# Kernel optimization log

Measured on AMD Instinct MI355X. Metric: run time of the kernel, lower is better.

The kernel has to match this reference:

```python
import jax, jax.numpy as jnp
import numpy as np

M, K, N = 8192, 4096, 12288


def setup_inputs() -> dict:
    key = jax.random.key(0)
    k1, k2, k3, k4 = jax.random.split(key, 4)
    input_tensor = jax.random.normal(k1, (1, M, K), dtype=jnp.float32)
    # int8 quantized weight [N, K] and per-output-channel scale [N, 1]
    weight = jax.random.randint(k2, (N, K), -127, 128, dtype=jnp.int32).astype(jnp.int8)
    weight_scale = (jax.random.uniform(k3, (N, 1), dtype=jnp.float32) * 0.01 + 1e-4)
    bias = jax.random.normal(k4, (N,), dtype=jnp.float32) * 0.1
    return {"input_tensor": input_tensor, "weight": weight,
            "weight_scale": weight_scale, "bias": bias}


def reference(input_tensor, weight, weight_scale, bias):
    x = input_tensor[0]  # squeeze(0) -> [M, K]
    # dynamic per-token symmetric int8 quantization: scale = absmax/127
    a_scale = jnp.max(jnp.abs(x), axis=-1, keepdims=True) / 127.0  # [M, 1]
    q = jnp.clip(jnp.round(x / a_scale), -128.0, 127.0)  # int8 values held in f32
    # int8 GEMM accumulated (emulated in f32), then dequant with per-token x per-channel scales
    acc = jnp.einsum('mk,nk->mn', q, weight.astype(jnp.float32))  # [M, N]
    out = acc * a_scale * weight_scale[:, 0][None, :] + bias[None, :]
    return out[None].astype(input_tensor.dtype)  # unsqueeze(0) -> [1, M, N]
```

## Files before the change

### kernel.cpp

```cpp
#include <hip/hip_runtime.h>
#include <cstdint>

#define M_DIM 8192
#define K_DIM 4096
#define N_DIM 12288
#define KT 64

using i32x4 = __attribute__((ext_vector_type(4))) int;

__device__ inline void gload_lds16(const void* g, void* l) {
    __builtin_amdgcn_global_load_lds(
        (const __attribute__((address_space(1))) void*)g,
        (__attribute__((address_space(3))) void*)l,
        16, 0, 0);
}

__global__ __launch_bounds__(256) void quant_pack(const float* __restrict__ x,
                                                  const int* __restrict__ w32,
                                                  int8_t* __restrict__ qa,
                                                  float* __restrict__ ascale,
                                                  int8_t* __restrict__ wq) {
    const int t = threadIdx.x;
    if (blockIdx.x < M_DIM) {
        const int row = blockIdx.x;
        const float4* xr = (const float4*)(x + (size_t)row * K_DIM);
        float4 v[4];
        float amax = 0.0f;
#pragma unroll
        for (int c = 0; c < 4; ++c) {
            v[c] = xr[t + 256 * c];
            amax = fmaxf(amax, fmaxf(fmaxf(fabsf(v[c].x), fabsf(v[c].y)),
                                     fmaxf(fabsf(v[c].z), fabsf(v[c].w))));
        }
#pragma unroll
        for (int off = 32; off > 0; off >>= 1)
            amax = fmaxf(amax, __shfl_xor(amax, off));
        __shared__ float smax[4];
        if ((t & 63) == 0) smax[t >> 6] = amax;
        __syncthreads();
        amax = fmaxf(fmaxf(smax[0], smax[1]), fmaxf(smax[2], smax[3]));
        const float sc = amax * (1.0f / 127.0f);
        const float inv = (amax > 0.0f) ? (127.0f / amax) : 0.0f;
        if (t == 0) ascale[row] = sc;

        int* q32 = (int*)(qa + (size_t)row * K_DIM);
#pragma unroll
        for (int c = 0; c < 4; ++c) {
            int q0 = (int)rintf(v[c].x * inv);
            int q1 = (int)rintf(v[c].y * inv);
            int q2 = (int)rintf(v[c].z * inv);
            int q3 = (int)rintf(v[c].w * inv);
            q0 = min(127, max(-128, q0));
            q1 = min(127, max(-128, q1));
            q2 = min(127, max(-128, q2));
            q3 = min(127, max(-128, q3));
            q32[t + 256 * c] = (q0 & 255) | ((q1 & 255) << 8) | ((q2 & 255) << 16) | (q3 << 24);
        }
    } else {
        const int pb = blockIdx.x - M_DIM;
        const size_t total4 = (size_t)N_DIM * K_DIM / 4;
        const size_t stride = (size_t)2048 * 256;
        int* out32 = (int*)wq;
        for (size_t i = (size_t)pb * 256 + t; i < total4; i += stride) {
            const int4 v = ((const int4*)w32)[i];
            out32[i] = (v.x & 255) | ((v.y & 255) << 8) | ((v.z & 255) << 16) | (v.w << 24);
        }
    }
}

__global__ __launch_bounds__(512, 2) void gemm_i8(const int8_t* __restrict__ qa,
                                                  const int8_t* __restrict__ wq,
                                                  const float* __restrict__ ascale,
                                                  const float* __restrict__ wscale,
                                                  const float* __restrict__ bias,
                                                  float* __restrict__ out) {
    __shared__ int8_t lds[4][2][16384];

    const int t = threadIdx.x;
    const int lane = t & 63;
    const int wave = t >> 6;
    const int wm = wave >> 2;
    const int wn = wave & 3;
    const int lrow = lane & 15;
    const int lk = lane >> 4;
    const int rslot = (lk ^ ((lrow >> 1) & 3)) << 4;

    const int flat = blockIdx.x;
    const int sw = (flat & 7) * 192 + (flat >> 3);
    const int bm = sw / 48;
    const int bn = sw % 48;

    const int g = (t & 3) ^ ((t >> 3) & 3);
    const size_t aoff0 = (size_t)(bm * 256 + (t >> 2)) * K_DIM + (size_t)g * 16;
    const size_t aoff1 = aoff0 + (size_t)128 * K_DIM;
    const size_t boff0 = (size_t)(bn * 256 + (t >> 2)) * K_DIM + (size_t)g * 16;
    const size_t boff1 = boff0 + (size_t)128 * K_DIM;

#define STAGE_A(sb, jt)                                                      \
    {                                                                        \
        gload_lds16(qa + aoff0 + (size_t)(jt) * 64, &lds[sb][0][t * 16]);    \
        gload_lds16(qa + aoff1 + (size_t)(jt) * 64,                          \
                    &lds[sb][0][t * 16 + 8192]);                             \
    }
#define STAGE_B(sb, jt)                                                      \
    {                                                                        \
        gload_lds16(wq + boff0 + (size_t)(jt) * 64, &lds[sb][1][t * 16]);    \
        gload_lds16(wq + boff1 + (size_t)(jt) * 64,                          \
                    &lds[sb][1][t * 16 + 8192]);                             \
    }

    i32x4 acc[8][4] = {};

#pragma unroll
    for (int p = 0; p < 3; ++p) {
        STAGE_A(p, p);
        STAGE_B(p, p);
    }

    for (int j = 0; j < KT; ++j) {
        const int cb = j & 3;
        const int pb = (j + 3) & 3;

        if (j + 3 < KT) {
            STAGE_A(pb, j + 3);
            asm volatile("s_waitcnt vmcnt(10)" ::: "memory");
        } else if (j + 2 < KT) {
            asm volatile("s_waitcnt vmcnt(8)" ::: "memory");
        } else if (j + 1 < KT) {
            asm volatile("s_waitcnt vmcnt(4)" ::: "memory");
        } else {
            asm volatile("s_waitcnt vmcnt(0)" ::: "memory");
        }
        __builtin_amdgcn_s_barrier();
        __builtin_amdgcn_sched_barrier(0);

        const int8_t* __restrict__ LA = lds[cb][0];
        const int8_t* __restrict__ LB = lds[cb][1];
        i32x4 af[4], bf[4], ah[4];
#pragma unroll
        for (int nf = 0; nf < 4; ++nf)
            bf[nf] = *(const i32x4*)&LB[(wn * 64 + nf * 16 + lrow) * 64 + rslot];
#pragma unroll
        for (int mf = 0; mf < 4; ++mf)
            af[mf] = *(const i32x4*)&LA[(wm * 128 + mf * 16 + lrow) * 64 + rslot];
        asm volatile("s_waitcnt lgkmcnt(0)" ::: "memory");
        __builtin_amdgcn_sched_barrier(0);
        __builtin_amdgcn_s_setprio(1);
#pragma unroll
        for (int mf = 0; mf < 4; ++mf)
#pragma unroll
            for (int nf = 0; nf < 4; ++nf)
                acc[mf][nf] = __builtin_amdgcn_mfma_i32_16x16x64_i8(
                    af[mf], bf[nf], acc[mf][nf], 0, 0, 0);
        __builtin_amdgcn_s_setprio(0);
        __builtin_amdgcn_s_barrier();

#pragma unroll
        for (int mf = 0; mf < 4; ++mf)
            ah[mf] = *(const i32x4*)&LA[(wm * 128 + (mf + 4) * 16 + lrow) * 64 + rslot];
        if (j + 3 < KT) STAGE_B(pb, j + 3);
        __builtin_amdgcn_s_barrier();
        asm volatile("s_waitcnt lgkmcnt(0)" ::: "memory");
        __builtin_amdgcn_sched_barrier(0);
        __builtin_amdgcn_s_setprio(1);
#pragma unroll
        for (int mf = 0; mf < 4; ++mf)
#pragma unroll
            for (int nf = 0; nf < 4; ++nf)
                acc[mf + 4][nf] = __builtin_amdgcn_mfma_i32_16x16x64_i8(
                    ah[mf], bf[nf], acc[mf + 4][nf], 0, 0, 0);
        __builtin_amdgcn_s_setprio(0);
        __builtin_amdgcn_s_barrier();
    }

    const int r0 = bm * 256 + wm * 128;
    const int c0 = bn * 256 + wn * 64;
    float asc[8][4];
#pragma unroll
    for (int m = 0; m < 8; ++m)
#pragma unroll
        for (int jj = 0; jj < 4; ++jj)
            asc[m][jj] = ascale[r0 + m * 16 + lk * 4 + jj];
#pragma unroll
    for (int n = 0; n < 4; ++n) {
        const int col = c0 + n * 16 + lrow;
        const float wsc = wscale[col];
        const float bb = bias[col];
#pragma unroll
        for (int m = 0; m < 8; ++m) {
#pragma unroll
            for (int jj = 0; jj < 4; ++jj) {
                const int row = r0 + m * 16 + lk * 4 + jj;
                out[(size_t)row * N_DIM + col] = (float)acc[m][n][jj] * asc[m][jj] * wsc + bb;
            }
        }
    }
}

extern "C" void kernel_launch(void* const* d_in, const int* in_sizes, int n_in,
                              void* d_out, int out_size, void* d_ws, size_t ws_size,
                              hipStream_t stream) {
    const float* x = (const float*)d_in[0];
    const int* w32 = (const int*)d_in[1];
    const float* wscale = (const float*)d_in[2];
    const float* bias = (const float*)d_in[3];
    float* out = (float*)d_out;

    int8_t* qa = (int8_t*)d_ws;
    float* ascale = (float*)((char*)d_ws + (size_t)M_DIM * K_DIM);
    int8_t* wq = (int8_t*)((char*)d_ws + (size_t)M_DIM * K_DIM +
                           (size_t)M_DIM * sizeof(float));

    quant_pack<<<M_DIM + 2048, 256, 0, stream>>>(x, w32, qa, ascale, wq);
    gemm_i8<<<1536, 512, 0, stream>>>(qa, wq, ascale, wscale, bias, out);
}
```

Baseline: 555.3 us.

## Double-buffer MFMA fragments in registers and prefetch next LDS tile during compute

Restructures the int8 GEMM main loop so the A and B fragments for the next K-tile are read from LDS into a second register set while the MFMAs run on the current set. All four global-to-LDS loads per tile are merged into one stage per iteration, and the loop is unrolled by two to alternate the register buffers. This cuts the barriers per K-step from four to one and hides LDS read latency behind MFMA work. The cost is more live VGPRs (two full 8x4 fragment sets alongside 128 accumulator registers), which under launch_bounds(512,2) risks spills or lower occupancy.

```diff
diff --git a/kernel.cpp b/kernel.cpp
--- a/kernel.cpp
+++ b/kernel.cpp
@@ -96,81 +96,71 @@
     const size_t boff0 = (size_t)(bn * 256 + (t >> 2)) * K_DIM + (size_t)g * 16;
     const size_t boff1 = boff0 + (size_t)128 * K_DIM;
 
-#define STAGE_A(sb, jt)                                                      \
-    {                                                                        \
-        gload_lds16(qa + aoff0 + (size_t)(jt) * 64, &lds[sb][0][t * 16]);    \
-        gload_lds16(qa + aoff1 + (size_t)(jt) * 64,                          \
-                    &lds[sb][0][t * 16 + 8192]);                             \
-    }
-#define STAGE_B(sb, jt)                                                      \
-    {                                                                        \
-        gload_lds16(wq + boff0 + (size_t)(jt) * 64, &lds[sb][1][t * 16]);    \
-        gload_lds16(wq + boff1 + (size_t)(jt) * 64,                          \
-                    &lds[sb][1][t * 16 + 8192]);                             \
+#define STAGE_ALL(sb, jt)                                                     \
+    {                                                                         \
+        gload_lds16(qa + aoff0 + (size_t)(jt) * 64, &lds[sb][0][t * 16]);     \
+        gload_lds16(qa + aoff1 + (size_t)(jt) * 64, &lds[sb][0][t * 16 + 8192]); \
+        gload_lds16(wq + boff0 + (size_t)(jt) * 64, &lds[sb][1][t * 16]);     \
+        gload_lds16(wq + boff1 + (size_t)(jt) * 64, &lds[sb][1][t * 16 + 8192]); \
     }
 
     i32x4 acc[8][4] = {};
-
-#pragma unroll
-    for (int p = 0; p < 3; ++p) {
-        STAGE_A(p, p);
-        STAGE_B(p, p);
-    }
-
-    for (int j = 0; j < KT; ++j) {
-        const int cb = j & 3;
-        const int pb = (j + 3) & 3;
-
-        if (j + 3 < KT) {
-            STAGE_A(pb, j + 3);
-            asm volatile("s_waitcnt vmcnt(10)" ::: "memory");
-        } else if (j + 2 < KT) {
-            asm volatile("s_waitcnt vmcnt(8)" ::: "memory");
-        } else if (j + 1 < KT) {
-            asm volatile("s_waitcnt vmcnt(4)" ::: "memory");
-        } else {
-            asm volatile("s_waitcnt vmcnt(0)" ::: "memory");
-        }
-        __builtin_amdgcn_s_barrier();
-        __builtin_amdgcn_sched_barrier(0);
-
-        const int8_t* __restrict__ LA = lds[cb][0];
-        const int8_t* __restrict__ LB = lds[cb][1];
-        i32x4 af[4], bf[4], ah[4];
+    i32x4 fa0[8], fb0[4], fa1[8], fb1[4];
+
+#pragma unroll
+    for (int p = 0; p < 3; ++p) STAGE_ALL(p, p);
+    asm volatile("s_waitcnt vmcnt(8)" ::: "memory");
+    __builtin_amdgcn_s_barrier();
+    __builtin_amdgcn_sched_barrier(0);
+    {
+        const int8_t* __restrict__ LA = lds[0][0];
+        const int8_t* __restrict__ LB = lds[0][1];
 #pragma unroll
         for (int nf = 0; nf < 4; ++nf)
-            bf[nf] = *(const i32x4*)&LB[(wn * 64 + nf * 16 + lrow) * 64 + rslot];
-#pragma unroll
-        for (int mf = 0; mf < 4; ++mf)
-            af[mf] = *(const i32x4*)&LA[(wm * 128 + mf * 16 + lrow) * 64 + rslot];
-        asm volatile("s_waitcnt lgkmcnt(0)" ::: "memory");
-        __builtin_amdgcn_sched_barrier(0);
-        __builtin_amdgcn_s_setprio(1);
-#pragma unroll
-        for (int mf = 0; mf < 4; ++mf)
-#pragma unroll
-            for (int nf = 0; nf < 4; ++nf)
-                acc[mf][nf] = __builtin_amdgcn_mfma_i32_16x16x64_i8(
-                    af[mf], bf[nf], acc[mf][nf], 0, 0, 0);
-        __builtin_amdgcn_s_setprio(0);
-        __builtin_amdgcn_s_barrier();
-
-#pragma unroll
-        for (int mf = 0; mf < 4; ++mf)
-            ah[mf] = *(const i32x4*)&LA[(wm * 128 + (mf + 4) * 16 + lrow) * 64 + rslot];
-        if (j + 3 < KT) STAGE_B(pb, j + 3);
-        __builtin_amdgcn_s_barrier();
-        asm volatile("s_waitcnt lgkmcnt(0)" ::: "memory");
-        __builtin_amdgcn_sched_barrier(0);
-        __builtin_amdgcn_s_setprio(1);
-#pragma unroll
-        for (int mf = 0; mf < 4; ++mf)
-#pragma unroll
-            for (int nf = 0; nf < 4; ++nf)
-                acc[mf + 4][nf] = __builtin_amdgcn_mfma_i32_16x16x64_i8(
-                    ah[mf], bf[nf], acc[mf + 4][nf], 0, 0, 0);
-        __builtin_amdgcn_s_setprio(0);
-        __builtin_amdgcn_s_barrier();
+            fb0[nf] = *(const i32x4*)&LB[(wn * 64 + nf * 16 + lrow) * 64 + rslot];
+#pragma unroll
+        for (int mf = 0; mf < 8; ++mf)
+            fa0[mf] = *(const i32x4*)&LA[(wm * 128 + mf * 16 + lrow) * 64 + rslot];
+    }
+
+#define ITER(J, CA, CB, NA, NB)                                               \
+    do {                                                                      \
+        if ((J) + 3 < KT) {                                                   \
+            STAGE_ALL(((J) + 3) & 3, (J) + 3);                                \
+            asm volatile("s_waitcnt vmcnt(8)" ::: "memory");                  \
+        } else if ((J) + 2 < KT) {                                            \
+            asm volatile("s_waitcnt vmcnt(4)" ::: "memory");                  \
+        } else if ((J) + 1 < KT) {                                            \
+            asm volatile("s_waitcnt vmcnt(0)" ::: "memory");                  \
+        }                                                                     \
+        __builtin_amdgcn_s_barrier();                                         \
+        __builtin_amdgcn_sched_barrier(0);                                    \
+        if ((J) + 1 < KT) {                                                   \
+            const int8_t* __restrict__ LA = lds[((J) + 1) & 3][0];            \
+            const int8_t* __restrict__ LB = lds[((J) + 1) & 3][1];            \
+            _Pragma("unroll")                                                 \
+            for (int nf = 0; nf < 4; ++nf)                                    \
+                NB[nf] = *(const i32x4*)&LB[(wn * 64 + nf * 16 + lrow) * 64 + rslot]; \
+            _Pragma("unroll")                                                 \
+            for (int mf = 0; mf < 8; ++mf)                                    \
+                NA[mf] = *(const i32x4*)&LA[(wm * 128 + mf * 16 + lrow) * 64 + rslot]; \
+        }                                                                     \
+        __builtin_amdgcn_sched_barrier(0);                                    \
+        __builtin_amdgcn_s_setprio(1);                                        \
+        _Pragma("unroll")                                                     \
+        for (int mf = 0; mf < 8; ++mf)                                        \
+            _Pragma("unroll")                                                 \
+            for (int nf = 0; nf < 4; ++nf)                                    \
+                acc[mf][nf] = __builtin_amdgcn_mfma_i32_16x16x64_i8(          \
+                    CA[mf], CB[nf], acc[mf][nf], 0, 0, 0);                    \
+        __builtin_amdgcn_s_setprio(0);                                        \
+        asm volatile("s_waitcnt lgkmcnt(0)" ::: "memory");                    \
+        __builtin_amdgcn_sched_barrier(0);                                    \
+    } while (0)
+
+    for (int j = 0; j < KT; j += 2) {
+        ITER(j, fa0, fb0, fa1, fb1);
+        ITER(j + 1, fa1, fb1, fa0, fb0);
     }
 
     const int r0 = bm * 256 + wm * 128;
```

Result: faster. 543.2 us (-2.2%).

## Switch int8 GEMM to K=128 tiles with double buffering and quadrant MFMA schedule

Applied to the files above, without the earlier changes.

Doubles the K-tile to 128 bytes and replaces the 4-stage, 64-wide LDS ring with a 2-stage double buffer of 128-wide tiles. It uses an 8-way XOR swizzle and splits each iteration into four quadrant MFMA phases that interleave LDS reads and global-to-LDS staging. The aim is fewer loop iterations and barriers per unit of K, and more MFMA work between synchronisations. In exchange, prefetch depth drops from three tiles to one, which may expose more global-memory latency.

```diff
diff --git a/kernel.cpp b/kernel.cpp
--- a/kernel.cpp
+++ b/kernel.cpp
@@ -4,7 +4,7 @@
 #define M_DIM 8192
 #define K_DIM 4096
 #define N_DIM 12288
-#define KT 64
+#define KT 32
 
 using i32x4 = __attribute__((ext_vector_type(4))) int;
 
@@ -74,7 +74,7 @@
                                                   const float* __restrict__ wscale,
                                                   const float* __restrict__ bias,
                                                   float* __restrict__ out) {
-    __shared__ int8_t lds[4][2][16384];
+    __shared__ int8_t lds[2][2][32768];
 
     const int t = threadIdx.x;
     const int lane = t & 63;
@@ -83,94 +83,95 @@
     const int wn = wave & 3;
     const int lrow = lane & 15;
     const int lk = lane >> 4;
-    const int rslot = (lk ^ ((lrow >> 1) & 3)) << 4;
+    const int sw7 = lrow & 7;
 
     const int flat = blockIdx.x;
     const int sw = (flat & 7) * 192 + (flat >> 3);
     const int bm = sw / 48;
     const int bn = sw % 48;
 
-    const int g = (t & 3) ^ ((t >> 3) & 3);
-    const size_t aoff0 = (size_t)(bm * 256 + (t >> 2)) * K_DIM + (size_t)g * 16;
-    const size_t aoff1 = aoff0 + (size_t)128 * K_DIM;
-    const size_t boff0 = (size_t)(bn * 256 + (t >> 2)) * K_DIM + (size_t)g * 16;
-    const size_t boff1 = boff0 + (size_t)128 * K_DIM;
-
-#define STAGE_A(sb, jt)                                                      \
-    {                                                                        \
-        gload_lds16(qa + aoff0 + (size_t)(jt) * 64, &lds[sb][0][t * 16]);    \
-        gload_lds16(qa + aoff1 + (size_t)(jt) * 64,                          \
-                    &lds[sb][0][t * 16 + 8192]);                             \
-    }
-#define STAGE_B(sb, jt)                                                      \
-    {                                                                        \
-        gload_lds16(wq + boff0 + (size_t)(jt) * 64, &lds[sb][1][t * 16]);    \
-        gload_lds16(wq + boff1 + (size_t)(jt) * 64,                          \
-                    &lds[sb][1][t * 16 + 8192]);                             \
-    }
+    const int srow = t >> 3;
+    const int g = (t & 7) ^ (srow & 7);
+
+#define STAGE_OP(ptr, sb, op, rowbase, jt)                                     \
+    {                                                                          \
+        _Pragma("unroll") for (int c = 0; c < 4; ++c)                          \
+            gload_lds16(ptr + (size_t)((rowbase) + srow + 64 * c) * K_DIM +    \
+                            (size_t)g * 16 + (size_t)(jt) * 128,               \
+                        &lds[sb][op][c * 8192 + t * 16]);                      \
+    }
+
+#define READ_A(dst, LA, mh)                                                    \
+    {                                                                          \
+        _Pragma("unroll") for (int mf = 0; mf < 4; ++mf)                       \
+            _Pragma("unroll") for (int ks = 0; ks < 2; ++ks)                   \
+                dst[mf][ks] = *(const i32x4*)&LA[(wm * 128 + (mh)*64 +         \
+                                                 mf * 16 + lrow) * 128 +       \
+                                                ((((ks << 2) | lk) ^ sw7) << 4)]; \
+    }
+#define READ_B(dst, LB, nh)                                                    \
+    {                                                                          \
+        _Pragma("unroll") for (int nf = 0; nf < 2; ++nf)                       \
+            _Pragma("unroll") for (int ks = 0; ks < 2; ++ks)                   \
+                dst[nf][ks] = *(const i32x4*)&LB[(wn * 64 + (nh)*32 +          \
+                                                 nf * 16 + lrow) * 128 +       \
+                                                ((((ks << 2) | lk) ^ sw7) << 4)]; \
+    }
+#define MM(AH, BH, mh, nh)                                                     \
+    {                                                                          \
+        __builtin_amdgcn_s_setprio(1);                                         \
+        _Pragma("unroll") for (int ks = 0; ks < 2; ++ks)                       \
+            _Pragma("unroll") for (int mf = 0; mf < 4; ++mf)                   \
+                _Pragma("unroll") for (int nf = 0; nf < 2; ++nf)               \
+                    acc[(mh)*4 + mf][(nh)*2 + nf] =                            \
+                        __builtin_amdgcn_mfma_i32_16x16x64_i8(                 \
+                            AH[mf][ks], BH[nf][ks],                            \
+                            acc[(mh)*4 + mf][(nh)*2 + nf], 0, 0, 0);           \
+        __builtin_amdgcn_s_setprio(0);                                         \
+    }
+#define LGKM0_PIN                                                              \
+    asm volatile("s_waitcnt lgkmcnt(0)" ::: "memory");                         \
+    __builtin_amdgcn_sched_barrier(0);
 
     i32x4 acc[8][4] = {};
-
-#pragma unroll
-    for (int p = 0; p < 3; ++p) {
-        STAGE_A(p, p);
-        STAGE_B(p, p);
-    }
+    i32x4 a0[4][2], a1[4][2], b0[2][2], b1[2][2];
+
+    STAGE_OP(qa, 0, 0, bm * 256, 0);
+    STAGE_OP(wq, 0, 1, bn * 256, 0);
 
     for (int j = 0; j < KT; ++j) {
-        const int cb = j & 3;
-        const int pb = (j + 3) & 3;
-
-        if (j + 3 < KT) {
-            STAGE_A(pb, j + 3);
-            asm volatile("s_waitcnt vmcnt(10)" ::: "memory");
-        } else if (j + 2 < KT) {
-            asm volatile("s_waitcnt vmcnt(8)" ::: "memory");
-        } else if (j + 1 < KT) {
+        const int cs = j & 1;
+        const int ns = cs ^ 1;
+        const int8_t* __restrict__ LA = lds[cs][0];
+        const int8_t* __restrict__ LB = lds[cs][1];
+
+        if (j + 1 < KT) {
+            STAGE_OP(qa, ns, 0, bm * 256, j + 1);
             asm volatile("s_waitcnt vmcnt(4)" ::: "memory");
         } else {
             asm volatile("s_waitcnt vmcnt(0)" ::: "memory");
         }
         __builtin_amdgcn_s_barrier();
         __builtin_amdgcn_sched_barrier(0);
-
-        const int8_t* __restrict__ LA = lds[cb][0];
-        const int8_t* __restrict__ LB = lds[cb][1];
-        i32x4 af[4], bf[4], ah[4];
-#pragma unroll
-        for (int nf = 0; nf < 4; ++nf)
-            bf[nf] = *(const i32x4*)&LB[(wn * 64 + nf * 16 + lrow) * 64 + rslot];
-#pragma unroll
-        for (int mf = 0; mf < 4; ++mf)
-            af[mf] = *(const i32x4*)&LA[(wm * 128 + mf * 16 + lrow) * 64 + rslot];
-        asm volatile("s_waitcnt lgkmcnt(0)" ::: "memory");
+        READ_A(a0, LA, 0);
+        READ_B(b0, LB, 0);
+        LGKM0_PIN;
+        MM(a0, b0, 0, 0);
+
+        READ_B(b1, LB, 1);
+        if (j + 1 < KT) STAGE_OP(wq, ns, 1, bn * 256, j + 1);
+        __builtin_amdgcn_s_barrier();
+        LGKM0_PIN;
+        MM(a0, b1, 0, 1);
+
+        READ_A(a1, LA, 1);
+        __builtin_amdgcn_s_barrier();
+        LGKM0_PIN;
+        MM(a1, b1, 1, 1);
+
+        __builtin_amdgcn_s_barrier();
         __builtin_amdgcn_sched_barrier(0);
-        __builtin_amdgcn_s_setprio(1);
-#pragma unroll
-        for (int mf = 0; mf < 4; ++mf)
-#pragma unroll
-            for (int nf = 0; nf < 4; ++nf)
-                acc[mf][nf] = __builtin_amdgcn_mfma_i32_16x16x64_i8(
-                    af[mf], bf[nf], acc[mf][nf], 0, 0, 0);
-        __builtin_amdgcn_s_setprio(0);
-        __builtin_amdgcn_s_barrier();
-
-#pragma unroll
-        for (int mf = 0; mf < 4; ++mf)
-            ah[mf] = *(const i32x4*)&LA[(wm * 128 + (mf + 4) * 16 + lrow) * 64 + rslot];
-        if (j + 3 < KT) STAGE_B(pb, j + 3);
-        __builtin_amdgcn_s_barrier();
-        asm volatile("s_waitcnt lgkmcnt(0)" ::: "memory");
-        __builtin_amdgcn_sched_barrier(0);
-        __builtin_amdgcn_s_setprio(1);
-#pragma unroll
-        for (int mf = 0; mf < 4; ++mf)
-#pragma unroll
-            for (int nf = 0; nf < 4; ++nf)
-                acc[mf + 4][nf] = __builtin_amdgcn_mfma_i32_16x16x64_i8(
-                    ah[mf], bf[nf], acc[mf + 4][nf], 0, 0, 0);
-        __builtin_amdgcn_s_setprio(0);
-        __builtin_amdgcn_s_barrier();
+        MM(a1, b0, 1, 0);
     }
 
     const int r0 = bm * 256 + wm * 128;
```

Result: faster. 503.5 us (-9.3%).

## Shrink GEMM tile to 128x128 with 4 waves and double-buffered LDS

Applied to the files above, without the earlier changes.

Replaces the 256x256 block tile with 8 waves and a 4-stage split-A/B pipeline with a 128x128 tile, 4 waves, and a simple 2-stage LDS double buffer. The grid grows from 1536 to 6144 blocks, with launch bounds set for 3 blocks per CU. The aim is higher occupancy and a simpler schedule. In exchange, each block reuses operands less, so global/L2 traffic per flop roughly doubles, and the prefetch depth is shallower.

```diff
diff --git a/kernel.cpp b/kernel.cpp
--- a/kernel.cpp
+++ b/kernel.cpp
@@ -68,116 +68,90 @@
     }
 }
 
-__global__ __launch_bounds__(512, 2) void gemm_i8(const int8_t* __restrict__ qa,
+__global__ __launch_bounds__(256, 3) void gemm_i8(const int8_t* __restrict__ qa,
                                                   const int8_t* __restrict__ wq,
                                                   const float* __restrict__ ascale,
                                                   const float* __restrict__ wscale,
                                                   const float* __restrict__ bias,
                                                   float* __restrict__ out) {
-    __shared__ int8_t lds[4][2][16384];
+    __shared__ int8_t lds[2][2][8192];
 
     const int t = threadIdx.x;
     const int lane = t & 63;
     const int wave = t >> 6;
-    const int wm = wave >> 2;
-    const int wn = wave & 3;
+    const int wm = wave >> 1;
+    const int wn = wave & 1;
     const int lrow = lane & 15;
     const int lk = lane >> 4;
     const int rslot = (lk ^ ((lrow >> 1) & 3)) << 4;
 
     const int flat = blockIdx.x;
-    const int sw = (flat & 7) * 192 + (flat >> 3);
-    const int bm = sw / 48;
-    const int bn = sw % 48;
+    const int sw = (flat & 7) * 768 + (flat >> 3);
+    const int bm = sw / 96;
+    const int bn = sw % 96;
 
     const int g = (t & 3) ^ ((t >> 3) & 3);
-    const size_t aoff0 = (size_t)(bm * 256 + (t >> 2)) * K_DIM + (size_t)g * 16;
-    const size_t aoff1 = aoff0 + (size_t)128 * K_DIM;
-    const size_t boff0 = (size_t)(bn * 256 + (t >> 2)) * K_DIM + (size_t)g * 16;
-    const size_t boff1 = boff0 + (size_t)128 * K_DIM;
+    const size_t aoff0 = (size_t)(bm * 128 + (t >> 2)) * K_DIM + (size_t)g * 16;
+    const size_t aoff1 = aoff0 + (size_t)64 * K_DIM;
+    const size_t boff0 = (size_t)(bn * 128 + (t >> 2)) * K_DIM + (size_t)g * 16;
+    const size_t boff1 = boff0 + (size_t)64 * K_DIM;
 
-#define STAGE_A(sb, jt)                                                      \
-    {                                                                        \
-        gload_lds16(qa + aoff0 + (size_t)(jt) * 64, &lds[sb][0][t * 16]);    \
-        gload_lds16(qa + aoff1 + (size_t)(jt) * 64,                          \
-                    &lds[sb][0][t * 16 + 8192]);                             \
-    }
-#define STAGE_B(sb, jt)                                                      \
-    {                                                                        \
-        gload_lds16(wq + boff0 + (size_t)(jt) * 64, &lds[sb][1][t * 16]);    \
-        gload_lds16(wq + boff1 + (size_t)(jt) * 64,                          \
-                    &lds[sb][1][t * 16 + 8192]);                             \
+#define STAGE(sb, jt)                                                          \
+    {                                                                          \
+        gload_lds16(qa + aoff0 + (size_t)(jt) * 64, &lds[sb][0][t * 16]);      \
+        gload_lds16(qa + aoff1 + (size_t)(jt) * 64, &lds[sb][0][t * 16 + 4096]); \
+        gload_lds16(wq + boff0 + (size_t)(jt) * 64, &lds[sb][1][t * 16]);      \
+        gload_lds16(wq + boff1 + (size_t)(jt) * 64, &lds[sb][1][t * 16 + 4096]); \
     }
 
-    i32x4 acc[8][4] = {};
+#define SB0 __builtin_amdgcn_sched_barrier(0);
+#define BAR __builtin_amdgcn_s_barrier();
+#define WAIT_LGKM(n) asm volatile("s_waitcnt lgkmcnt(" #n ")" ::: "memory");
+#define WAIT_VM(n) asm volatile("s_waitcnt vmcnt(" #n ")" ::: "memory");
 
-#pragma unroll
-    for (int p = 0; p < 3; ++p) {
-        STAGE_A(p, p);
-        STAGE_B(p, p);
-    }
+    i32x4 acc[4][4] = {};
+    i32x4 a[4], b[4];
+
+    STAGE(0, 0);
 
     for (int j = 0; j < KT; ++j) {
-        const int cb = j & 3;
-        const int pb = (j + 3) & 3;
-
-        if (j + 3 < KT) {
-            STAGE_A(pb, j + 3);
-            asm volatile("s_waitcnt vmcnt(10)" ::: "memory");
-        } else if (j + 2 < KT) {
-            asm volatile("s_waitcnt vmcnt(8)" ::: "memory");
-        } else if (j + 1 < KT) {
-            asm volatile("s_waitcnt vmcnt(4)" ::: "memory");
+        const int cs = j & 1;
+        const int ns = cs ^ 1;
+        if (j + 1 < KT) {
+            STAGE(ns, j + 1);
+            WAIT_VM(4);
         } else {
-            asm volatile("s_waitcnt vmcnt(0)" ::: "memory");
+            WAIT_VM(0);
         }
-        __builtin_amdgcn_s_barrier();
-        __builtin_amdgcn_sched_barrier(0);
-
-        const int8_t* __restrict__ LA = lds[cb][0];
-        const int8_t* __restrict__ LB = lds[cb][1];
-        i32x4 af[4], bf[4], ah[4];
+        SB0;
+        BAR;
+        SB0;
 #pragma unroll
         for (int nf = 0; nf < 4; ++nf)
-            bf[nf] = *(const i32x4*)&LB[(wn * 64 + nf * 16 + lrow) * 64 + rslot];
+            b[nf] = *(const i32x4*)&lds[cs][1][(wn * 64 + nf * 16 + lrow) * 64 + rslot];
 #pragma unroll
         for (int mf = 0; mf < 4; ++mf)
-            af[mf] = *(const i32x4*)&LA[(wm * 128 + mf * 16 + lrow) * 64 + rslot];
-        asm volatile("s_waitcnt lgkmcnt(0)" ::: "memory");
-        __builtin_amdgcn_sched_barrier(0);
+            a[mf] = *(const i32x4*)&lds[cs][0][(wm * 64 + mf * 16 + lrow) * 64 + rslot];
+        WAIT_LGKM(0);
+        SB0;
+        BAR;
+        SB0;
         __builtin_amdgcn_s_setprio(1);
 #pragma unroll
         for (int mf = 0; mf < 4; ++mf)
 #pragma unroll
             for (int nf = 0; nf < 4; ++nf)
                 acc[mf][nf] = __builtin_amdgcn_mfma_i32_16x16x64_i8(
-                    af[mf], bf[nf], acc[mf][nf], 0, 0, 0);
+                    a[mf], b[nf], acc[mf][nf], 0, 0, 0);
         __builtin_amdgcn_s_setprio(0);
-        __builtin_amdgcn_s_barrier();
-
-#pragma unroll
-        for (int mf = 0; mf < 4; ++mf)
-            ah[mf] = *(const i32x4*)&LA[(wm * 128 + (mf + 4) * 16 + lrow) * 64 + rslot];
-        if (j + 3 < KT) STAGE_B(pb, j + 3);
-        __builtin_amdgcn_s_barrier();
-        asm volatile("s_waitcnt lgkmcnt(0)" ::: "memory");
-        __builtin_amdgcn_sched_barrier(0);
-        __builtin_amdgcn_s_setprio(1);
-#pragma unroll
-        for (int mf = 0; mf < 4; ++mf)
-#pragma unroll
-            for (int nf = 0; nf < 4; ++nf)
-                acc[mf + 4][nf] = __builtin_amdgcn_mfma_i32_16x16x64_i8(
-                    ah[mf], bf[nf], acc[mf + 4][nf], 0, 0, 0);
-        __builtin_amdgcn_s_setprio(0);
-        __builtin_amdgcn_s_barrier();
+        SB0;
     }
 
-    const int r0 = bm * 256 + wm * 128;
-    const int c0 = bn * 256 + wn * 64;
-    float asc[8][4];
+    const int r0 = bm * 128 + wm * 64;
+    const int c0 = bn * 128 + wn * 64;
+    float asc[4][4];
 #pragma unroll
-    for (int m = 0; m < 8; ++m)
+    for (int m = 0; m < 4; ++m)
 #pragma unroll
         for (int jj = 0; jj < 4; ++jj)
             asc[m][jj] = ascale[r0 + m * 16 + lk * 4 + jj];
@@ -187,7 +161,7 @@
         const float wsc = wscale[col];
         const float bb = bias[col];
 #pragma unroll
-        for (int m = 0; m < 8; ++m) {
+        for (int m = 0; m < 4; ++m) {
 #pragma unroll
             for (int jj = 0; jj < 4; ++jj) {
                 const int row = r0 + m * 16 + lk * 4 + jj;
@@ -212,5 +186,5 @@
                            (size_t)M_DIM * sizeof(float));
 
     quant_pack<<<M_DIM + 2048, 256, 0, stream>>>(x, w32, qa, ascale, wq);
-    gemm_i8<<<1536, 512, 0, stream>>>(qa, wq, ascale, wscale, bias, out);
+    gemm_i8<<<6144, 256, 0, stream>>>(qa, wq, ascale, wscale, bias, out);
 }
```

Result: slower. 663.9 us (+19.6%).
